# Kernel tuning notes

Measured on AMD Instinct MI355X. Metric: run time of the kernel, lower is better.

The kernel has to match this reference:

```python
import jax, jax.numpy as jnp
import numpy as np

B, N, C, S = 2, 250000, 32, 128


def setup_inputs() -> dict:
    key = jax.random.key(0)
    k1, k2, k3, k4 = jax.random.split(key, 4)
    # unique voxel coordinates per batch (spconv requires unique active sites)
    rng = np.random.default_rng(0)
    coords = []
    for b in range(B):
        lin = rng.choice(S * S * S, size=N, replace=False)
        x = lin // (S * S)
        y = (lin // S) % S
        z = lin % S
        coords.append(np.stack([x, y, z], axis=-1))
    coordinates = jnp.asarray(np.stack(coords, axis=0), dtype=jnp.int32)  # [B,N,3]
    features = jax.random.normal(k1, (B, N, C), dtype=jnp.float32)
    wscale = 1.0 / np.sqrt(27 * C)
    W1 = jax.random.normal(k2, (3, 3, 3, C, C), dtype=jnp.float32) * wscale
    W2 = jax.random.normal(k3, (3, 3, 3, C, C), dtype=jnp.float32) * wscale
    W3 = jax.random.normal(k4, (3, 3, 3, C, C), dtype=jnp.float32) * wscale
    return {
        "features": features,
        "coordinates": coordinates,
        "spatial_shape": jnp.array([S, S, S], dtype=jnp.int32),
        "batch_size": B,
        "W1": W1,
        "W2": W2,
        "W3": W3,
    }


def reference(features, coordinates, spatial_shape, batch_size, W1, W2, W3):
    Bs = int(batch_size)
    X, Y, Z = [int(s) for s in np.asarray(spatial_shape)]
    n = coordinates.shape[1]
    M = Bs * n
    cin = features.shape[-1]
    b_idx = jnp.repeat(jnp.arange(Bs, dtype=jnp.int32), n)  # [M]
    coords = coordinates.reshape(-1, 3).astype(jnp.int32)  # [M,3]
    feat = features.reshape(-1, cin)  # [M,Cin]
    # dense hash grid: voxel -> row index in feat, -1 if inactive
    grid = jnp.full((Bs, X, Y, Z), -1, dtype=jnp.int32)
    grid = grid.at[b_idx, coords[:, 0], coords[:, 1], coords[:, 2]].set(
        jnp.arange(M, dtype=jnp.int32))

    cx, cy, cz = coords[:, 0], coords[:, 1], coords[:, 2]

    def subm_conv(f, W):
        # submanifold 3x3x3 conv: output only at active sites, gather active
        # neighbors (rulebook gather -> GEMM -> accumulate)
        cout = W.shape[-1]
        out = jnp.zeros((M, cout), dtype=f.dtype)
        for dx in range(3):
            for dy in range(3):
                for dz in range(3):
                    nx, ny, nz = cx + dx - 1, cy + dy - 1, cz + dz - 1
                    valid = ((nx >= 0) & (nx < X) & (ny >= 0) & (ny < Y)
                             & (nz >= 0) & (nz < Z))
                    idx = grid[b_idx,
                               jnp.clip(nx, 0, X - 1),
                               jnp.clip(ny, 0, Y - 1),
                               jnp.clip(nz, 0, Z - 1)]
                    idx = jnp.where(valid, idx, -1)
                    g = jnp.where((idx >= 0)[:, None],
                                  f[jnp.maximum(idx, 0)], 0.0)
                    out = out + g @ W[dx, dy, dz]
        return out

    x = jax.nn.relu(subm_conv(feat, W1))
    x = jax.nn.relu(subm_conv(x, W2))
    x = subm_conv(x, W3)
    return x.reshape(Bs, n, -1)
```

## Files before the change

### kernel.cpp

```cpp
#include <hip/hip_runtime.h>

#define SG 128
#define C 32
#define NPB 250000
#define BATCH 2
#define M (BATCH * NPB)
#define MP 500032
#define NW (MP / 64)
#define NK 27
#define NBKT 65536
#define CAP 256
#define HSZ 1024

typedef __attribute__((ext_vector_type(4))) float f32x4;
typedef __attribute__((ext_vector_type(8))) short bf16x8;

union frag_u { unsigned u[4]; bf16x8 v; };

__device__ __forceinline__ int bucket_key(int b, int x, int y, int z) {
    return (b << 15) | ((x >> 2) << 10) | ((y >> 2) << 5) | (z >> 2);
}

__device__ __forceinline__ void gl_lds16(const void* g, void* l) {
    __builtin_amdgcn_global_load_lds(
        (const __attribute__((address_space(1))) unsigned int*)g,
        (__attribute__((address_space(3))) unsigned int*)l, 16, 0, 0);
}

__global__ void hist_kernel(const int* __restrict__ coords, int* __restrict__ hist) {
    int p = blockIdx.x * blockDim.x + threadIdx.x;
    if (p >= M) return;
    int x = coords[3 * p + 0], y = coords[3 * p + 1], z = coords[3 * p + 2];
    atomicAdd(&hist[bucket_key(p >= NPB, x, y, z)], 1);
}

__global__ __launch_bounds__(256) void scan_kernel(int* __restrict__ h) {
    __shared__ int part[256];
    int t = threadIdx.x;
    int s = 0;
    for (int i = 0; i < 256; i++) s += h[t * 256 + i];
    part[t] = s;
    __syncthreads();
    if (t == 0) {
        int run = 0;
        for (int i = 0; i < 256; i++) { int v = part[i]; part[i] = run; run += v; }
    }
    __syncthreads();
    int run = part[t];
    for (int i = 0; i < 256; i++) { int v = h[t * 256 + i]; h[t * 256 + i] = run; run += v; }
}

__global__ void place_kernel(const int* __restrict__ coords, int* __restrict__ h,
                             int* __restrict__ ord, int* __restrict__ gridP) {
    int p = blockIdx.x * blockDim.x + threadIdx.x;
    if (p >= M) return;
    int x = coords[3 * p + 0], y = coords[3 * p + 1], z = coords[3 * p + 2];
    int b = (p >= NPB) ? 1 : 0;
    int j = atomicAdd(&h[bucket_key(b, x, y, z)], 1);
    ord[j] = p;
    gridP[((b * SG + x) * SG + y) * SG + z] = j;
}

__global__ __launch_bounds__(64) void build_dedup_kernel(
    const int* __restrict__ coords, const int* __restrict__ ord,
    const int* __restrict__ gridP,
    unsigned short* __restrict__ nbL, int* __restrict__ uniq, int* __restrict__ ucnt)
{
    __shared__ int hkey[HSZ];
    __shared__ int hval[HSZ];
    __shared__ int hcnt;
    const int t = threadIdx.x;
    const int w = blockIdx.x;
    for (int i = t; i < HSZ; i += 64) { hkey[i] = -2; hval[i] = -1; }
    if (t == 0) { hcnt = 1; uniq[w * CAP] = -1; }
    __syncthreads();

    const int j = w * 64 + t;
    int x = 0, y = 0, z = 0, base = 0;
    const bool real = (j < M);
    if (real) {
        int p = ord[j];
        x = coords[3 * p + 0]; y = coords[3 * p + 1]; z = coords[3 * p + 2];
        base = (p >= NPB) ? SG * SG * SG : 0;
    }
    for (int k = 0; k < NK; k++) {
        int id = -1;
        if (real) {
            int nx = x + k / 9 - 1;
            int ny = y + (k / 3) % 3 - 1;
            int nz = z + (k % 3) - 1;
            if ((unsigned)nx < SG && (unsigned)ny < SG && (unsigned)nz < SG)
                id = gridP[base + (nx * SG + ny) * SG + nz];
        }
        int slot = 0;
        if (id >= 0) {
            unsigned h = (((unsigned)id * 2654435761u) >> 20) & (HSZ - 1);
            slot = -1;
            while (slot < 0) {
                int old = atomicCAS(&hkey[h], -2, id);
                bool won = (old == -2);
                int myslot = -1;
                if (won) myslot = atomicAdd(&hcnt, 1);
                if (won) {
                    if (myslot < CAP) { hval[h] = myslot; uniq[w * CAP + myslot] = id; slot = myslot; }
                    else { hval[h] = 0; slot = 0; }
                } else if (old == id) {
                    int v = hval[h];
                    if (v >= 0) slot = v;
                } else {
                    h = (h + 1) & (HSZ - 1);
                }
            }
        }
        nbL[((size_t)w * NK + k) * 64 + (t & 15) * 4 + (t >> 4)] = (unsigned short)slot;
    }
    __syncthreads();
    if (t == 0) ucnt[w] = (hcnt < CAP) ? hcnt : CAP;
}

__global__ void prep_w_kernel(const float* __restrict__ W, unsigned short* __restrict__ wpk) {
    int id = blockIdx.x * blockDim.x + threadIdx.x;
    if (id >= NK * 2 * 64) return;
    int l = id & 63, ct = (id >> 6) & 1, k = id >> 7;
    int lrow = l & 15, kg = l >> 4;
    unsigned hw[4], lw[4];
#pragma unroll
    for (int jp = 0; jp < 4; jp++) {
        float v0 = W[k * 1024 + (kg * 8 + 2 * jp + 0) * 32 + ct * 16 + lrow];
        float v1 = W[k * 1024 + (kg * 8 + 2 * jp + 1) * 32 + ct * 16 + lrow];
        unsigned u0 = __float_as_uint(v0), u1 = __float_as_uint(v1);
        hw[jp] = (u0 >> 16) | (u1 & 0xFFFF0000u);
        float h0 = __uint_as_float(u0 & 0xFFFF0000u);
        float h1 = __uint_as_float(u1 & 0xFFFF0000u);
        lw[jp] = (__float_as_uint(v0 - h0) >> 16) | (__float_as_uint(v1 - h1) & 0xFFFF0000u);
    }
    unsigned* dh = (unsigned*)(wpk + k * 2048 + ((ct * 2 + 0) * 64 + l) * 8);
    unsigned* dl = (unsigned*)(wpk + k * 2048 + ((ct * 2 + 1) * 64 + l) * 8);
#pragma unroll
    for (int i = 0; i < 4; i++) { dh[i] = hw[i]; dl[i] = lw[i]; }
}

__device__ __forceinline__ void split1(float v, unsigned short& h, unsigned short& lo) {
    unsigned u = __float_as_uint(v);
    h = (unsigned short)(u >> 16);
    float hf = __uint_as_float(u & 0xFFFF0000u);
    lo = (unsigned short)(__float_as_uint(v - hf) >> 16);
}

__global__ void split_in_kernel(const float* __restrict__ f, const int* __restrict__ ord,
                                unsigned short* __restrict__ fpk) {
    int id = blockIdx.x * blockDim.x + threadIdx.x;
    if (id >= M * 8) return;
    int j = id >> 3, c4 = id & 7;
    int p = ord[j];
    f32x4 v = *(const f32x4*)&f[p * 32 + c4 * 4];
    ushort4 h, lo;
    split1(v[0], h.x, lo.x);
    split1(v[1], h.y, lo.y);
    split1(v[2], h.z, lo.z);
    split1(v[3], h.w, lo.w);
    *(ushort4*)&fpk[j * 64 + c4 * 4] = h;
    *(ushort4*)&fpk[j * 64 + 32 + c4 * 4] = lo;
}

template <bool RELU, bool LAST>
__global__ __launch_bounds__(256) void conv_mfma(
    const unsigned short* __restrict__ fpk,
    const unsigned short* __restrict__ nbL,
    const int* __restrict__ uniq,
    const int* __restrict__ ucnt,
    const unsigned short* __restrict__ wpk,
    const unsigned short* __restrict__ zrow,
    const int* __restrict__ ord,
    unsigned short* __restrict__ opk,
    float* __restrict__ of32)
{
    __shared__ char bufA[CAP * 128];

    const int t = threadIdx.x;
    const int l = t & 63;
    const int wv = t >> 6;
    const int lrow = l & 15, kg = l >> 4;
    const int w = blockIdx.x;
    const int wbase = w * 64;

    const int lane_r = l >> 3;
    const int lc = l & 7;
    {
        const int cnt = ucnt[w];
        char* ldsb = bufA + wv * 64 * 128;
#pragma unroll
        for (int i = 0; i < 8; i++) {
            int r = wv * 64 + i * 8 + lane_r;
            int id = (r < cnt) ? uniq[(size_t)w * CAP + r] : -1;
            const unsigned short* src = (id >= 0)
                ? fpk + (size_t)id * 64 + ((lc ^ lane_r) << 3)
                : zrow + (lc << 3);
            gl_lds16(src, ldsb + i * 1024);
        }
    }

    const int kbeg = wv * 7;
    const int ntap = (wv == 3) ? 6 : 7;
    ushort4 q[7];
#pragma unroll
    for (int i = 0; i < 7; i++) {
        int k = kbeg + i; if (k > 26) k = 26;
        q[i] = *(const ushort4*)(nbL + ((size_t)w * NK + k) * 64 + lrow * 4);
    }
    __builtin_amdgcn_sched_barrier(0);
    __syncthreads();

    f32x4 acc[4][2];
#pragma unroll
    for (int rt = 0; rt < 4; rt++)
#pragma unroll
        for (int ct = 0; ct < 2; ct++) acc[rt][ct] = (f32x4){0.f, 0.f, 0.f, 0.f};

#pragma unroll
    for (int i = 0; i < 7; i++) {
        if (i < ntap) {
            const int k = kbeg + i;
            const unsigned short* wb = wpk + (k << 11);
            frag_u w0, w1, w2, w3;
            w0.v = *(const bf16x8*)(wb + ((0 * 64 + l) << 3));
            w1.v = *(const bf16x8*)(wb + ((1 * 64 + l) << 3));
            w2.v = *(const bf16x8*)(wb + ((2 * 64 + l) << 3));
            w3.v = *(const bf16x8*)(wb + ((3 * 64 + l) << 3));
            int rows[4] = {q[i].x & 255, q[i].y & 255, q[i].z & 255, q[i].w & 255};
            frag_u ah[4], al[4];
#pragma unroll
            for (int rt = 0; rt < 4; rt++) {
                int r = rows[rt];
                const char* rb = bufA + (r << 7);
                int sw = (r & 7) << 4;
                ah[rt].v = *(const bf16x8*)(rb + ((kg << 4) ^ sw));
                al[rt].v = *(const bf16x8*)(rb + (((kg + 4) << 4) ^ sw));
            }
#pragma unroll
            for (int rt = 0; rt < 4; rt++) {
                acc[rt][0] = __builtin_amdgcn_mfma_f32_16x16x32_bf16(ah[rt].v, w0.v, acc[rt][0], 0, 0, 0);
                acc[rt][1] = __builtin_amdgcn_mfma_f32_16x16x32_bf16(ah[rt].v, w2.v, acc[rt][1], 0, 0, 0);
                acc[rt][0] = __builtin_amdgcn_mfma_f32_16x16x32_bf16(ah[rt].v, w1.v, acc[rt][0], 0, 0, 0);
                acc[rt][1] = __builtin_amdgcn_mfma_f32_16x16x32_bf16(ah[rt].v, w3.v, acc[rt][1], 0, 0, 0);
                acc[rt][0] = __builtin_amdgcn_mfma_f32_16x16x32_bf16(al[rt].v, w0.v, acc[rt][0], 0, 0, 0);
                acc[rt][1] = __builtin_amdgcn_mfma_f32_16x16x32_bf16(al[rt].v, w2.v, acc[rt][1], 0, 0, 0);
            }
        }
    }
    __syncthreads();

    f32x4* dmp = (f32x4*)bufA;
#pragma unroll
    for (int rt = 0; rt < 4; rt++)
#pragma unroll
        for (int ct = 0; ct < 2; ct++)
            dmp[((wv * 8 + rt * 2 + ct) << 6) + l] = acc[rt][ct];
    __syncthreads();

    f32x4 fin[2] = {(f32x4){0.f, 0.f, 0.f, 0.f}, (f32x4){0.f, 0.f, 0.f, 0.f}};
#pragma unroll
    for (int s = 0; s < 4; s++)
#pragma unroll
        for (int ct = 0; ct < 2; ct++)
            fin[ct] += dmp[((s * 8 + wv * 2 + ct) << 6) + l];

    const int rbase = wbase + wv * 16 + 4 * kg;
#pragma unroll
    for (int j = 0; j < 4; j++) {
        int row = rbase + j;
        if (row < M) {
            int orow = LAST ? ord[row] : row;
#pragma unroll
            for (int ct = 0; ct < 2; ct++) {
                int col = ct * 16 + lrow;
                float v = fin[ct][j];
                if (RELU) v = fmaxf(v, 0.f);
                if (LAST) {
                    of32[orow * 32 + col] = v;
                } else {
                    unsigned short h, lo;
                    split1(v, h, lo);
                    opk[row * 64 + col] = h;
                    opk[row * 64 + 32 + col] = lo;
                }
            }
        }
    }
}

extern "C" void kernel_launch(void* const* d_in, const int* in_sizes, int n_in,
                              void* d_out, int out_size, void* d_ws, size_t ws_size,
                              hipStream_t stream) {
    const float* features    = (const float*)d_in[0];
    const int*   coordinates = (const int*)d_in[1];
    const float* W1 = (const float*)d_in[4];
    const float* W2 = (const float*)d_in[5];
    const float* W3 = (const float*)d_in[6];

    char* ws = (char*)d_ws;
    const size_t GRID_BYTES = (size_t)BATCH * SG * SG * SG * 4;
    const size_t NBL_BYTES  = (size_t)NW * NK * 64 * 2;
    const size_t UNIQ_BYTES = (size_t)NW * CAP * 4;
    const size_t UCNT_BYTES = (size_t)NW * 4;
    const size_t HIST_BYTES = (size_t)NBKT * 4;
    const size_t ORD_BYTES  = (size_t)MP * 4;
    const size_t WPK_BYTES  = (size_t)NK * 2048 * 2;
    const size_t Z_BYTES    = 256;

    size_t off = 0;
    int* gridP = (int*)(ws + off); off += GRID_BYTES;
    unsigned short* nbL = (unsigned short*)(ws + off); off += NBL_BYTES;
    int* uniq  = (int*)(ws + off); off += UNIQ_BYTES;
    int* ucnt  = (int*)(ws + off); off += UCNT_BYTES;
    int* hist  = (int*)(ws + off); off += HIST_BYTES;
    int* ord   = (int*)(ws + off); off += ORD_BYTES;
    unsigned short* wpk1 = (unsigned short*)(ws + off); off += WPK_BYTES;
    unsigned short* wpk2 = (unsigned short*)(ws + off); off += WPK_BYTES;
    unsigned short* wpk3 = (unsigned short*)(ws + off); off += WPK_BYTES;
    unsigned short* zrow = (unsigned short*)(ws + off); off += Z_BYTES;
    unsigned short* fpk_a = (unsigned short*)(ws + off); off += (size_t)MP * 64 * 2;
    unsigned short* fpk_b = (unsigned short*)d_out;
    float* out = (float*)d_out;

    hipMemsetAsync(gridP, 0xFF, GRID_BYTES, stream);
    hipMemsetAsync(hist, 0, HIST_BYTES, stream);
    hipMemsetAsync(zrow, 0, Z_BYTES, stream);

    hist_kernel<<<(M + 255) / 256, 256, 0, stream>>>(coordinates, hist);
    scan_kernel<<<1, 256, 0, stream>>>(hist);
    place_kernel<<<(M + 255) / 256, 256, 0, stream>>>(coordinates, hist, ord, gridP);
    build_dedup_kernel<<<NW, 64, 0, stream>>>(coordinates, ord, gridP, nbL, uniq, ucnt);

    const int PW = NK * 2 * 64;
    prep_w_kernel<<<(PW + 255) / 256, 256, 0, stream>>>(W1, wpk1);
    prep_w_kernel<<<(PW + 255) / 256, 256, 0, stream>>>(W2, wpk2);
    prep_w_kernel<<<(PW + 255) / 256, 256, 0, stream>>>(W3, wpk3);

    split_in_kernel<<<(M * 8 + 255) / 256, 256, 0, stream>>>(features, ord, fpk_a);

    conv_mfma<true,  false><<<NW, 256, 0, stream>>>(fpk_a, nbL, uniq, ucnt, wpk1, zrow, ord, fpk_b, nullptr);
    conv_mfma<true,  false><<<NW, 256, 0, stream>>>(fpk_b, nbL, uniq, ucnt, wpk2, zrow, ord, fpk_a, nullptr);
    conv_mfma<false, true ><<<NW, 256, 0, stream>>>(fpk_a, nbL, uniq, ucnt, wpk3, zrow, ord, nullptr, out);
}
```

Before: 419.1 us.

## Split conv work across waves by output rows instead of kernel taps

Each wave now owns 16 output rows and loops over all 27 taps, where before each wave took a subset of taps over all 64 rows. That removes the LDS partial-sum dump, the extra barriers and the cross-wave reduction. The per-block neighbor table is staged into shared memory so each lane can read its row index per tap. In exchange every wave now loads weights for all 27 taps, so weight traffic per wave grows, and the MFMA chain per tap is shorter, which may expose more latency.

```diff
diff --git a/kernel.cpp b/kernel.cpp
--- a/kernel.cpp
+++ b/kernel.cpp
@@ -176,6 +176,7 @@
     float* __restrict__ of32)
 {
     __shared__ char bufA[CAP * 128];
+    __shared__ unsigned short smS[NK * 64];
 
     const int t = threadIdx.x;
     const int l = t & 63;
@@ -199,71 +200,43 @@
             gl_lds16(src, ldsb + i * 1024);
         }
     }
-
-    const int kbeg = wv * 7;
-    const int ntap = (wv == 3) ? 6 : 7;
-    ushort4 q[7];
-#pragma unroll
-    for (int i = 0; i < 7; i++) {
-        int k = kbeg + i; if (k > 26) k = 26;
-        q[i] = *(const ushort4*)(nbL + ((size_t)w * NK + k) * 64 + lrow * 4);
+    {
+        const unsigned* sb = (const unsigned*)(nbL + (size_t)w * NK * 64);
+        unsigned* ds = (unsigned*)smS;
+#pragma unroll
+        for (int i = 0; i < 4; i++) {
+            int d = t + i * 256;
+            if (d < 864) ds[d] = sb[d];
+        }
     }
     __builtin_amdgcn_sched_barrier(0);
     __syncthreads();
 
-    f32x4 acc[4][2];
-#pragma unroll
-    for (int rt = 0; rt < 4; rt++)
-#pragma unroll
-        for (int ct = 0; ct < 2; ct++) acc[rt][ct] = (f32x4){0.f, 0.f, 0.f, 0.f};
-
-#pragma unroll
-    for (int i = 0; i < 7; i++) {
-        if (i < ntap) {
-            const int k = kbeg + i;
-            const unsigned short* wb = wpk + (k << 11);
-            frag_u w0, w1, w2, w3;
-            w0.v = *(const bf16x8*)(wb + ((0 * 64 + l) << 3));
-            w1.v = *(const bf16x8*)(wb + ((1 * 64 + l) << 3));
-            w2.v = *(const bf16x8*)(wb + ((2 * 64 + l) << 3));
-            w3.v = *(const bf16x8*)(wb + ((3 * 64 + l) << 3));
-            int rows[4] = {q[i].x & 255, q[i].y & 255, q[i].z & 255, q[i].w & 255};
-            frag_u ah[4], al[4];
-#pragma unroll
-            for (int rt = 0; rt < 4; rt++) {
-                int r = rows[rt];
-                const char* rb = bufA + (r << 7);
-                int sw = (r & 7) << 4;
-                ah[rt].v = *(const bf16x8*)(rb + ((kg << 4) ^ sw));
-                al[rt].v = *(const bf16x8*)(rb + (((kg + 4) << 4) ^ sw));
-            }
-#pragma unroll
-            for (int rt = 0; rt < 4; rt++) {
-                acc[rt][0] = __builtin_amdgcn_mfma_f32_16x16x32_bf16(ah[rt].v, w0.v, acc[rt][0], 0, 0, 0);
-                acc[rt][1] = __builtin_amdgcn_mfma_f32_16x16x32_bf16(ah[rt].v, w2.v, acc[rt][1], 0, 0, 0);
-                acc[rt][0] = __builtin_amdgcn_mfma_f32_16x16x32_bf16(ah[rt].v, w1.v, acc[rt][0], 0, 0, 0);
-                acc[rt][1] = __builtin_amdgcn_mfma_f32_16x16x32_bf16(ah[rt].v, w3.v, acc[rt][1], 0, 0, 0);
-                acc[rt][0] = __builtin_amdgcn_mfma_f32_16x16x32_bf16(al[rt].v, w0.v, acc[rt][0], 0, 0, 0);
-                acc[rt][1] = __builtin_amdgcn_mfma_f32_16x16x32_bf16(al[rt].v, w2.v, acc[rt][1], 0, 0, 0);
-            }
-        }
-    }
-    __syncthreads();
-
-    f32x4* dmp = (f32x4*)bufA;
-#pragma unroll
-    for (int rt = 0; rt < 4; rt++)
-#pragma unroll
-        for (int ct = 0; ct < 2; ct++)
-            dmp[((wv * 8 + rt * 2 + ct) << 6) + l] = acc[rt][ct];
-    __syncthreads();
-
-    f32x4 fin[2] = {(f32x4){0.f, 0.f, 0.f, 0.f}, (f32x4){0.f, 0.f, 0.f, 0.f}};
-#pragma unroll
-    for (int s = 0; s < 4; s++)
-#pragma unroll
-        for (int ct = 0; ct < 2; ct++)
-            fin[ct] += dmp[((s * 8 + wv * 2 + ct) << 6) + l];
+    f32x4 acc0 = (f32x4){0.f, 0.f, 0.f, 0.f};
+    f32x4 acc1 = (f32x4){0.f, 0.f, 0.f, 0.f};
+    const unsigned short* srow = smS + lrow * 4 + wv;
+
+#pragma unroll
+    for (int k = 0; k < NK; k++) {
+        const int r = srow[k * 64];
+        const unsigned short* wb = wpk + (k << 11);
+        frag_u w0, w1, w2, w3;
+        w0.v = *(const bf16x8*)(wb + ((0 * 64 + l) << 3));
+        w1.v = *(const bf16x8*)(wb + ((1 * 64 + l) << 3));
+        w2.v = *(const bf16x8*)(wb + ((2 * 64 + l) << 3));
+        w3.v = *(const bf16x8*)(wb + ((3 * 64 + l) << 3));
+        frag_u ah, al;
+        const char* rb = bufA + (r << 7);
+        const int sw = (r & 7) << 4;
+        ah.v = *(const bf16x8*)(rb + ((kg << 4) ^ sw));
+        al.v = *(const bf16x8*)(rb + (((kg + 4) << 4) ^ sw));
+        acc0 = __builtin_amdgcn_mfma_f32_16x16x32_bf16(ah.v, w0.v, acc0, 0, 0, 0);
+        acc1 = __builtin_amdgcn_mfma_f32_16x16x32_bf16(ah.v, w2.v, acc1, 0, 0, 0);
+        acc0 = __builtin_amdgcn_mfma_f32_16x16x32_bf16(ah.v, w1.v, acc0, 0, 0, 0);
+        acc1 = __builtin_amdgcn_mfma_f32_16x16x32_bf16(ah.v, w3.v, acc1, 0, 0, 0);
+        acc0 = __builtin_amdgcn_mfma_f32_16x16x32_bf16(al.v, w0.v, acc0, 0, 0, 0);
+        acc1 = __builtin_amdgcn_mfma_f32_16x16x32_bf16(al.v, w2.v, acc1, 0, 0, 0);
+    }
 
     const int rbase = wbase + wv * 16 + 4 * kg;
 #pragma unroll
@@ -274,7 +247,7 @@
 #pragma unroll
             for (int ct = 0; ct < 2; ct++) {
                 int col = ct * 16 + lrow;
-                float v = fin[ct][j];
+                float v = ct ? acc1[j] : acc0[j];
                 if (RELU) v = fmaxf(v, 0.f);
                 if (LAST) {
                     of32[orow * 32 + col] = v;
```

Result: slower. 585.4 us (+39.7%).
